# Kernel optimization log

Measured on AMD Instinct MI355X. Metric: run time of the kernel, lower is better.

Reference implementation:

```python
import jax, jax.numpy as jnp
import numpy as np

TILE = 8

def _dct_mat():
    # D[k, n] = cos(pi/N * (n + 0.5) * k), matches gen_filters(8,8,dct_coeff)
    k = np.arange(TILE)[:, None]
    n = np.arange(TILE)[None, :]
    return jnp.asarray(np.cos(np.pi / TILE * (n + 0.5) * k), dtype=jnp.float32)

def _idct_mat():
    # ID[k, n] = ((n==0)*(-1/2) + cos(pi/N*(k+0.5)*n)) * sqrt(1/(2N))
    k = np.arange(TILE)[:, None]
    n = np.arange(TILE)[None, :]
    m = ((n == 0) * (-0.5) + np.cos(np.pi / TILE * (k + 0.5) * n)) * np.sqrt(1.0 / (2.0 * TILE))
    return jnp.asarray(m, dtype=jnp.float32)

def _zigzag_tile(keep_count):
    mask = np.zeros((TILE, TILE), dtype=np.float32)
    order = sorted(((x, y) for x in range(TILE) for y in range(TILE)),
                   key=lambda p: (p[0] + p[1], -p[1] if (p[0] + p[1]) % 2 else p[1]))
    for i, j in order[:keep_count]:
        mask[i, j] = 1.0
    return mask

def _yuv_mask(H, W, keeps=(25, 9, 9)):
    chans = []
    for kc in keeps:
        t = _zigzag_tile(kc)
        full = np.tile(t, (int(np.ceil(H / TILE)), int(np.ceil(W / TILE))))[:H, :W]
        chans.append(full)
    return jnp.asarray(np.stack(chans, axis=0), dtype=jnp.float32)  # [3,H,W]

# rgb2yuv / yuv2rgb matrices from the source
_RGB2YUV = jnp.asarray([[0.299, 0.587, 0.114],
                        [-0.14713, -0.28886, 0.436],
                        [0.615, -0.51499, -0.10001]], dtype=jnp.float32)
_YUV2RGB = jnp.asarray([[1.0, 0.0, 1.13983],
                        [1.0, -0.39465, -0.5806],
                        [1.0, 2.03211, 0.0]], dtype=jnp.float32)

def _block_transform(x, M):
    # x: [B,C,H,W]; per non-overlapping 8x8 tile: out = M @ tile @ M^T
    B, C, H, W = x.shape
    xb = x.reshape(B, C, H // TILE, TILE, W // TILE, TILE)
    yb = jnp.einsum('kn,lm,bcinjm->bcikjl', M, M, xb)
    return yb.reshape(B, C, H, W)

def setup_inputs() -> dict:
    key = jax.random.key(0)
    steg = jax.random.normal(key, (16, 3, 512, 512), dtype=jnp.float32)
    return {"steg": steg}

def reference(steg) -> jnp.ndarray:
    B, C, H, W = steg.shape
    pad_h = (TILE - H % TILE) % TILE
    pad_w = (TILE - W % TILE) % TILE
    x = jnp.pad(steg, ((0, 0), (0, 0), (0, pad_h), (0, pad_w)))
    Hp, Wp = H + pad_h, W + pad_w
    # colorspace convert: [B,3,H,W]
    yuv = jnp.einsum('oc,bchw->bohw', _RGB2YUV, x)
    # blockwise DCT, zigzag mask, blockwise IDCT
    dct = _block_transform(yuv, _dct_mat())
    mask = _yuv_mask(Hp, Wp)  # [3,Hp,Wp]
    dct_masked = dct * mask[None]
    idct = _block_transform(dct_masked, _idct_mat())
    rgb = jnp.einsum('oc,bchw->bohw', _YUV2RGB, idct)
    return rgb[:, :, :H, :W]
```

## Files before the change

### kernel.cpp

```cpp
#include <hip/hip_runtime.h>
#include <cstdint>
#include <cstddef>

namespace {

constexpr int TIL = 8;
constexpr int WID = 512;
constexpr int HEI = 512;
constexpr int NB  = 16;
constexpr int TPR = WID / TIL;
constexpr int LSTRIDE = 65;
constexpr int CH = TPR * LSTRIDE;

constexpr float C16[17] = {
  1.0f, 0.9807852804032304f, 0.9238795325112867f, 0.8314696123025452f,
  0.7071067811865476f, 0.5555702330196022f, 0.3826834323650898f,
  0.1950903220161283f, 0.0f, -0.1950903220161283f, -0.3826834323650898f,
  -0.5555702330196022f, -0.7071067811865476f, -0.8314696123025452f,
  -0.9238795325112867f, -0.9807852804032304f, -1.0f
};

constexpr float cosp(int t) {
  int a = ((t % 32) + 32) % 32;
  return (a <= 16) ? C16[a] : C16[32 - a];
}

struct Tbl { float D[8][8]; float ID[8][8]; };

constexpr Tbl make_tbl() {
  Tbl t{};
  for (int k = 0; k < 8; ++k)
    for (int n = 0; n < 8; ++n) {
      t.D[k][n] = cosp((2 * n + 1) * k);
      float v = cosp((2 * k + 1) * n);
      if (n == 0) v -= 0.5f;
      t.ID[k][n] = v * 0.25f;
    }
  return t;
}

constexpr Tbl TBL = make_tbl();

constexpr bool keptY(int k, int l) { return (k + l <= 5) || (k + l == 6 && l <= 3); }
constexpr bool keptC(int k, int l) { return (k + l <= 2) || (k + l == 3 && k <= 2); }

template <bool ISY>
__device__ __forceinline__ void tile_transform(float* __restrict__ t) {
  constexpr int KM = ISY ? 7 : 3;

  float T[KM][8];
#pragma unroll
  for (int k = 0; k < KM; ++k)
#pragma unroll
    for (int m = 0; m < 8; ++m) T[k][m] = 0.0f;

#pragma unroll
  for (int n = 0; n < 8; ++n) {
    float x[8];
#pragma unroll
    for (int m = 0; m < 8; ++m) x[m] = t[n * 8 + m];
#pragma unroll
    for (int k = 0; k < KM; ++k) {
      const float d = TBL.D[k][n];
#pragma unroll
      for (int m = 0; m < 8; ++m) T[k][m] += d * x[m];
    }
  }

  float Yv[KM][8];
#pragma unroll
  for (int k = 0; k < KM; ++k)
#pragma unroll
    for (int l = 0; l < 8; ++l) {
      const bool kept = ISY ? keptY(k, l) : keptC(k, l);
      if (kept) {
        float s = 0.0f;
#pragma unroll
        for (int m = 0; m < 8; ++m) s += T[k][m] * TBL.D[l][m];
        Yv[k][l] = s;
      }
    }

  float Uv[KM][8];
#pragma unroll
  for (int k = 0; k < KM; ++k)
#pragma unroll
    for (int q = 0; q < 8; ++q) {
      float s = 0.0f;
#pragma unroll
      for (int l = 0; l < 8; ++l) {
        const bool kept = ISY ? keptY(k, l) : keptC(k, l);
        if (kept) s += Yv[k][l] * TBL.ID[q][l];
      }
      Uv[k][q] = s;
    }

#pragma unroll
  for (int p = 0; p < 8; ++p)
#pragma unroll
    for (int q = 0; q < 8; ++q) {
      float s = 0.0f;
#pragma unroll
      for (int k = 0; k < KM; ++k) s += TBL.ID[p][k] * Uv[k][q];
      t[p * 8 + q] = s;
    }
}

__global__ __launch_bounds__(256) void jpeg_kernel(const float* __restrict__ in,
                                                   float* __restrict__ out) {
  __shared__ float lds[3 * CH];
  const int tid = threadIdx.x;
  const int blk = blockIdx.x;
  const int b  = blk >> 6;
  const int ti = blk & 63;
  const size_t plane = (size_t)HEI * WID;
  const size_t base0 = (size_t)b * 3 * plane + (size_t)(ti * TIL) * WID;

#pragma unroll
  for (int it = 0; it < 4; ++it) {
    const int p4  = it * 256 + tid;
    const int row = p4 >> 7;
    const int col = (p4 & 127) << 2;
    const size_t g = base0 + (size_t)row * WID + col;
    const float4 rq = *(const float4*)(in + g);
    const float4 gq = *(const float4*)(in + g + plane);
    const float4 bq = *(const float4*)(in + g + 2 * plane);
    const int off = (col >> 3) * LSTRIDE + row * 8 + (col & 7);
    const float rr[4] = {rq.x, rq.y, rq.z, rq.w};
    const float gg[4] = {gq.x, gq.y, gq.z, gq.w};
    const float bb[4] = {bq.x, bq.y, bq.z, bq.w};
#pragma unroll
    for (int j = 0; j < 4; ++j) {
      const float R = rr[j], G = gg[j], Bv = bb[j];
      lds[          off + j] =  0.299f   * R + 0.587f   * G + 0.114f   * Bv;
      lds[CH      + off + j] = -0.14713f * R - 0.28886f * G + 0.436f   * Bv;
      lds[2 * CH  + off + j] =  0.615f   * R - 0.51499f * G - 0.10001f * Bv;
    }
  }
  __syncthreads();

  if (tid < 192) {
    const int c = tid >> 6;
    float* tp = lds + c * CH + (tid & 63) * LSTRIDE;
    if (c == 0) tile_transform<true>(tp);
    else        tile_transform<false>(tp);
  }
  __syncthreads();

#pragma unroll
  for (int it = 0; it < 4; ++it) {
    const int p4  = it * 256 + tid;
    const int row = p4 >> 7;
    const int col = (p4 & 127) << 2;
    const int off = (col >> 3) * LSTRIDE + row * 8 + (col & 7);
    float4 ro, go, bo;
#pragma unroll
    for (int j = 0; j < 4; ++j) {
      const float Yy = lds[         off + j];
      const float Uu = lds[CH     + off + j];
      const float Vv = lds[2 * CH + off + j];
      (&ro.x)[j] = Yy + 1.13983f * Vv;
      (&go.x)[j] = Yy - 0.39465f * Uu - 0.5806f * Vv;
      (&bo.x)[j] = Yy + 2.03211f * Uu;
    }
    const size_t g = base0 + (size_t)row * WID + col;
    *(float4*)(out + g)             = ro;
    *(float4*)(out + g + plane)     = go;
    *(float4*)(out + g + 2 * plane) = bo;
  }
}

}

extern "C" void kernel_launch(void* const* d_in, const int* in_sizes, int n_in,
                              void* d_out, int out_size, void* d_ws, size_t ws_size,
                              hipStream_t stream) {
  const float* in = (const float*)d_in[0];
  float* out = (float*)d_out;
  jpeg_kernel<<<dim3(NB * (HEI / TIL)), dim3(256), 0, stream>>>(in, out);
}
```

Measured before the change: 98.82 us.

## Vectorize LDS accesses, batch global loads, and use nontemporal stores

Changes the LDS tile stride to an even value so each tile row can be read and written with float2 accesses instead of scalars. All twelve global float4 loads are issued before any YUV conversion, so more memory requests are in flight at once. Output stores become nontemporal to avoid polluting the cache, and the tile transform uses explicit FMAs with the row and column passes fused per k. The wider LDS accesses may bring back bank conflicts that the odd stride of 65 was chosen to avoid, and batching the loads raises register pressure.

```diff
diff --git a/kernel.cpp b/kernel.cpp
--- a/kernel.cpp
+++ b/kernel.cpp
@@ -9,8 +9,10 @@
 constexpr int HEI = 512;
 constexpr int NB  = 16;
 constexpr int TPR = WID / TIL;
-constexpr int LSTRIDE = 65;
+constexpr int LSTRIDE = 66;
 constexpr int CH = TPR * LSTRIDE;
+
+typedef float vf4 __attribute__((ext_vector_type(4)));
 
 constexpr float C16[17] = {
   1.0f, 0.9807852804032304f, 0.9238795325112867f, 0.8314696123025452f,
@@ -58,52 +60,56 @@
   for (int n = 0; n < 8; ++n) {
     float x[8];
 #pragma unroll
-    for (int m = 0; m < 8; ++m) x[m] = t[n * 8 + m];
+    for (int h = 0; h < 4; ++h) {
+      const float2 v = ((const float2*)(t + n * 8))[h];
+      x[2 * h] = v.x; x[2 * h + 1] = v.y;
+    }
 #pragma unroll
     for (int k = 0; k < KM; ++k) {
       const float d = TBL.D[k][n];
 #pragma unroll
-      for (int m = 0; m < 8; ++m) T[k][m] += d * x[m];
-    }
-  }
-
-  float Yv[KM][8];
-#pragma unroll
-  for (int k = 0; k < KM; ++k)
+      for (int m = 0; m < 8; ++m) T[k][m] = __builtin_fmaf(d, x[m], T[k][m]);
+    }
+  }
+
+  float Uv[KM][8];
+#pragma unroll
+  for (int k = 0; k < KM; ++k) {
+    float yv[8];
 #pragma unroll
     for (int l = 0; l < 8; ++l) {
-      const bool kept = ISY ? keptY(k, l) : keptC(k, l);
-      if (kept) {
+      if (ISY ? keptY(k, l) : keptC(k, l)) {
         float s = 0.0f;
 #pragma unroll
-        for (int m = 0; m < 8; ++m) s += T[k][m] * TBL.D[l][m];
-        Yv[k][l] = s;
+        for (int m = 0; m < 8; ++m) s = __builtin_fmaf(T[k][m], TBL.D[l][m], s);
+        yv[l] = s;
       }
     }
-
-  float Uv[KM][8];
-#pragma unroll
-  for (int k = 0; k < KM; ++k)
 #pragma unroll
     for (int q = 0; q < 8; ++q) {
       float s = 0.0f;
 #pragma unroll
-      for (int l = 0; l < 8; ++l) {
-        const bool kept = ISY ? keptY(k, l) : keptC(k, l);
-        if (kept) s += Yv[k][l] * TBL.ID[q][l];
-      }
+      for (int l = 0; l < 8; ++l)
+        if (ISY ? keptY(k, l) : keptC(k, l))
+          s = __builtin_fmaf(yv[l], TBL.ID[q][l], s);
       Uv[k][q] = s;
     }
-
-#pragma unroll
-  for (int p = 0; p < 8; ++p)
+  }
+
+#pragma unroll
+  for (int p = 0; p < 8; ++p) {
+    float o[8];
 #pragma unroll
     for (int q = 0; q < 8; ++q) {
       float s = 0.0f;
 #pragma unroll
-      for (int k = 0; k < KM; ++k) s += TBL.ID[p][k] * Uv[k][q];
-      t[p * 8 + q] = s;
-    }
+      for (int k = 0; k < KM; ++k) s = __builtin_fmaf(TBL.ID[p][k], Uv[k][q], s);
+      o[q] = s;
+    }
+#pragma unroll
+    for (int h = 0; h < 4; ++h)
+      ((float2*)(t + p * 8))[h] = make_float2(o[2 * h], o[2 * h + 1]);
+  }
 }
 
 __global__ __launch_bounds__(256) void jpeg_kernel(const float* __restrict__ in,
@@ -116,26 +122,39 @@
   const size_t plane = (size_t)HEI * WID;
   const size_t base0 = (size_t)b * 3 * plane + (size_t)(ti * TIL) * WID;
 
+  float4 rq[4], gq[4], bq[4];
+  int offv[4];
 #pragma unroll
   for (int it = 0; it < 4; ++it) {
     const int p4  = it * 256 + tid;
     const int row = p4 >> 7;
     const int col = (p4 & 127) << 2;
     const size_t g = base0 + (size_t)row * WID + col;
-    const float4 rq = *(const float4*)(in + g);
-    const float4 gq = *(const float4*)(in + g + plane);
-    const float4 bq = *(const float4*)(in + g + 2 * plane);
-    const int off = (col >> 3) * LSTRIDE + row * 8 + (col & 7);
-    const float rr[4] = {rq.x, rq.y, rq.z, rq.w};
-    const float gg[4] = {gq.x, gq.y, gq.z, gq.w};
-    const float bb[4] = {bq.x, bq.y, bq.z, bq.w};
+    rq[it] = *(const float4*)(in + g);
+    gq[it] = *(const float4*)(in + g + plane);
+    bq[it] = *(const float4*)(in + g + 2 * plane);
+    offv[it] = (col >> 3) * LSTRIDE + row * 8 + (col & 7);
+  }
+#pragma unroll
+  for (int it = 0; it < 4; ++it) {
+    const float rr[4] = {rq[it].x, rq[it].y, rq[it].z, rq[it].w};
+    const float gg[4] = {gq[it].x, gq[it].y, gq[it].z, gq[it].w};
+    const float bb[4] = {bq[it].x, bq[it].y, bq[it].z, bq[it].w};
+    float y[4], u[4], v[4];
 #pragma unroll
     for (int j = 0; j < 4; ++j) {
       const float R = rr[j], G = gg[j], Bv = bb[j];
-      lds[          off + j] =  0.299f   * R + 0.587f   * G + 0.114f   * Bv;
-      lds[CH      + off + j] = -0.14713f * R - 0.28886f * G + 0.436f   * Bv;
-      lds[2 * CH  + off + j] =  0.615f   * R - 0.51499f * G - 0.10001f * Bv;
-    }
+      y[j] =  0.299f   * R + 0.587f   * G + 0.114f   * Bv;
+      u[j] = -0.14713f * R - 0.28886f * G + 0.436f   * Bv;
+      v[j] =  0.615f   * R - 0.51499f * G - 0.10001f * Bv;
+    }
+    const int off = offv[it];
+    ((float2*)(lds + off))[0]          = make_float2(y[0], y[1]);
+    ((float2*)(lds + off))[1]          = make_float2(y[2], y[3]);
+    ((float2*)(lds + CH + off))[0]     = make_float2(u[0], u[1]);
+    ((float2*)(lds + CH + off))[1]     = make_float2(u[2], u[3]);
+    ((float2*)(lds + 2 * CH + off))[0] = make_float2(v[0], v[1]);
+    ((float2*)(lds + 2 * CH + off))[1] = make_float2(v[2], v[3]);
   }
   __syncthreads();
 
@@ -153,20 +172,23 @@
     const int row = p4 >> 7;
     const int col = (p4 & 127) << 2;
     const int off = (col >> 3) * LSTRIDE + row * 8 + (col & 7);
-    float4 ro, go, bo;
-#pragma unroll
-    for (int j = 0; j < 4; ++j) {
-      const float Yy = lds[         off + j];
-      const float Uu = lds[CH     + off + j];
-      const float Vv = lds[2 * CH + off + j];
-      (&ro.x)[j] = Yy + 1.13983f * Vv;
-      (&go.x)[j] = Yy - 0.39465f * Uu - 0.5806f * Vv;
-      (&bo.x)[j] = Yy + 2.03211f * Uu;
+    vf4 ro, go, bo;
+#pragma unroll
+    for (int h = 0; h < 2; ++h) {
+      const float2 yy = ((const float2*)(lds + off))[h];
+      const float2 uu = ((const float2*)(lds + CH + off))[h];
+      const float2 vv = ((const float2*)(lds + 2 * CH + off))[h];
+      ro[2 * h]     = yy.x + 1.13983f * vv.x;
+      ro[2 * h + 1] = yy.y + 1.13983f * vv.y;
+      go[2 * h]     = yy.x - 0.39465f * uu.x - 0.5806f * vv.x;
+      go[2 * h + 1] = yy.y - 0.39465f * uu.y - 0.5806f * vv.y;
+      bo[2 * h]     = yy.x + 2.03211f * uu.x;
+      bo[2 * h + 1] = yy.y + 2.03211f * uu.y;
     }
     const size_t g = base0 + (size_t)row * WID + col;
-    *(float4*)(out + g)             = ro;
-    *(float4*)(out + g + plane)     = go;
-    *(float4*)(out + g + 2 * plane) = bo;
+    __builtin_nontemporal_store(ro, (vf4*)(out + g));
+    __builtin_nontemporal_store(go, (vf4*)(out + g + plane));
+    __builtin_nontemporal_store(bo, (vf4*)(out + g + 2 * plane));
   }
 }
 
```

New measurement: 97.32 us. Within noise of the previous version (-1.5%).
